# Optimization experiments

Hardware: AMD Instinct MI355X
Metric: run time of the kernel (lower is better)

The kernel has to match this reference:

```python
import jax, jax.numpy as jnp
import numpy as np

# Standard genetic code: 64 codons ordered by bases T,C,A,G (first/second/third position).
AA64 = "FFLLSSSSYY**CC*WLLLLPPPPHHQQRRRRIIIMTTTTNNKKSSRRVVVVAAAADDEEGGGG"
NC = 65  # codon vocab: id 0 = PAD, ids 1..64 = codons
_uniq = sorted(set(AA64))
_gid = {a: i + 1 for i, a in enumerate(_uniq)}          # group 0 reserved for PAD
NG = len(_uniq) + 1                                      # number of AA groups (+dummy)
GROUP_IDS = jnp.asarray(np.array([0] + [_gid[a] for a in AA64], dtype=np.int32))
IS_CODING = jnp.asarray(np.array([False] + [a != '*' for a in AA64]))
_syn = {a: AA64.count(a) for a in _uniq}
NSYN = jnp.asarray(np.array([0.0] + [float(_syn[a]) for a in AA64], dtype=np.float32))

LOSS_W = dict(ce=1.0, cai=0.4, rscu=0.3, gc=0.1, structure=0.15, dynamics=0.1)
EPS = 1e-8


def _cai(codon_ids, species_ids, mask, weight_matrix):
    # per-token gather of CAI weights: [B, L]
    w = weight_matrix[species_ids[:, None], codon_ids]
    log_w = jnp.log(jnp.maximum(w, EPS))
    m = mask.astype(log_w.dtype)
    mean_log = (log_w * m).sum(1) / jnp.maximum(m.sum(1), 1.0)
    return jnp.exp(mean_log)  # [B]


def _seq_rscu(codon_ids, aa_ids, mask):
    # grouped codon histogram -> RSCU: count * n_syn(aa) / total_count(aa)
    B = codon_ids.shape[0]
    bi = jnp.arange(B)[:, None]
    valid = mask & (codon_ids > 0)
    counts = jnp.zeros((B, NC), jnp.float32).at[bi, codon_ids].add(valid.astype(jnp.float32))
    aa_valid = valid & (aa_ids > 2)  # positions with a real amino-acid token
    observed = jnp.zeros((B, NC), jnp.float32).at[bi, codon_ids].add(aa_valid.astype(jnp.float32)) > 0
    observed = observed & IS_CODING[None, :]
    obs_counts = counts * observed  # counts of codons observed under a valid AA
    # segment-sum over synonymous-codon groups
    group_sum = jnp.zeros((B, NG), jnp.float32).at[:, GROUP_IDS].add(obs_counts)
    tot = group_sum[:, GROUP_IDS]  # [B, NC] total count of each codon's syn group
    return jnp.where(observed & (tot > 0), obs_counts * NSYN[None, :] / jnp.maximum(tot, 1.0), 0.0)


def _rscu_kl(pred_ids, target_ids, aa_ids, species_ids, mask, ref_distributions):
    pred_rscu = _seq_rscu(pred_ids, aa_ids, mask)
    target_rscu = _seq_rscu(target_ids, aa_ids, mask)
    ref_rscu = ref_distributions[species_ids]  # [B, NC]
    combined = 0.7 * target_rscu + 0.3 * ref_rscu + EPS
    pred = pred_rscu + EPS
    p = pred / pred.sum(1, keepdims=True)
    t = combined / combined.sum(1, keepdims=True)
    return (t * (jnp.log(t) - jnp.log(p))).sum(1)  # [B]


def setup_inputs() -> dict:
    key = jax.random.key(0)
    ks = jax.random.split(key, 9)
    B, L = 64, 8192
    return {
        "logits": jax.random.normal(ks[0], (B, L, NC), jnp.float32),
        "weight_matrix": jax.random.uniform(ks[1], (5, NC), jnp.float32),
        "ref_distributions": jax.random.uniform(ks[2], (5, NC), jnp.float32) * 2.0,
        "gc_pred": jax.random.uniform(ks[3], (B, L), jnp.float32),
        "mfe": jax.random.normal(ks[4], (B,), jnp.float32) * 5.0 - 20.0,
        "pause_prob": jax.random.uniform(ks[5], (B, L), jnp.float32),
        "target_codon_ids": jax.random.randint(ks[6], (B, L), 0, NC),
        "aa_ids": jax.random.randint(ks[7], (B, L), 0, 25),
        "species_ids": jax.random.randint(ks[8], (B,), 0, 5),
        "mask": jnp.ones((B, L), dtype=bool),
    }


def reference(logits, weight_matrix, ref_distributions, gc_pred, mfe, pause_prob,
              target_codon_ids, aa_ids, species_ids, mask):
    # CE with ignore_index=0
    logp = jax.nn.log_softmax(logits, axis=-1)
    nll = -jnp.take_along_axis(logp, target_codon_ids[..., None], axis=-1)[..., 0]
    v = (target_codon_ids != 0).astype(logits.dtype)
    ce = (nll * v).sum() / jnp.maximum(v.sum(), 1.0)

    pred_ids = jnp.argmax(logits, axis=-1)

    pred_cai = _cai(pred_ids, species_ids, mask, weight_matrix)
    target_cai = _cai(target_codon_ids, species_ids, mask, weight_matrix)
    cai_loss = jax.nn.relu(target_cai - pred_cai).mean()

    rscu_loss = _rscu_kl(pred_ids, target_codon_ids, aa_ids, species_ids, mask, ref_distributions).mean()

    gc_loss = jnp.mean((gc_pred.mean(1) - 0.5) ** 2)
    structure_loss = jnp.mean((mfe - (-20.0)) ** 2)
    dynamics_loss = jnp.mean((pause_prob.mean(1) - 0.1) ** 2)

    total = (LOSS_W['ce'] * ce + LOSS_W['cai'] * cai_loss + LOSS_W['rscu'] * rscu_loss
             + LOSS_W['gc'] * gc_loss + LOSS_W['structure'] * structure_loss
             + LOSS_W['dynamics'] * dynamics_loss)
    return total
```

## Files before the change

kernel.cpp:

```cpp
#include <hip/hip_runtime.h>
#include <math.h>
#include <stdint.h>

#define NCC 65
#define NGG 22
#define BB  64
#define LL  8192
#define EPSF 1e-8f
#define TPB 128
#define PPB 128
#define TILES 4
#define SUBS 16
#define NBLK (BB * SUBS)

__device__ __constant__ int c_gid[NCC] = {0,
  6,6,11,11,17,17,17,17,21,21,1,1,3,3,1,20,
  11,11,11,11,14,14,14,14,8,8,15,15,16,16,16,16,
  9,9,9,12,18,18,18,18,13,13,10,10,17,17,16,16,
  19,19,19,19,2,2,2,2,4,4,5,5,7,7,7,7};
__device__ __constant__ int c_coding[NCC] = {0,
  1,1,1,1,1,1,1,1,1,1,0,0,1,1,0,1,
  1,1,1,1,1,1,1,1,1,1,1,1,1,1,1,1,
  1,1,1,1,1,1,1,1,1,1,1,1,1,1,1,1,
  1,1,1,1,1,1,1,1,1,1,1,1,1,1,1,1};
__device__ __constant__ float c_nsyn[NCC] = {0.f,
  2,2,6,6,6,6,6,6,2,2,3,3,2,2,3,1,
  6,6,6,6,4,4,4,4,2,2,2,2,6,6,6,6,
  3,3,3,1,4,4,4,4,2,2,2,2,6,6,6,6,
  4,4,4,4,4,4,4,4,2,2,2,2,4,4,4,4};

#define WS_NLL  0
#define WS_VC   64
#define WS_LWP  128
#define WS_LWT  192
#define WS_G    256
#define WS_P    320
#define WS_PART 384
#define WS_HIST 448

__global__ __launch_bounds__(TPB) void k_main(
    const float* __restrict__ logits, const float* __restrict__ wmat,
    const float* __restrict__ gcp,    const float* __restrict__ ppr,
    const int* __restrict__ tgt,      const int* __restrict__ aa,
    const int* __restrict__ spec,     float* __restrict__ ws)
{
  const int b    = blockIdx.x >> 4;
  const int sub  = blockIdx.x & (SUBS - 1);
  const int tid  = threadIdx.x;
  const int lane = tid & 63;

  __shared__ float tile[PPB * NCC];
  __shared__ float lwrow[NCC];
  __shared__ int hPV[NCC], hPA[NCC], hTV[NCC], hTA[NCC];

  const int sp = spec[b];
  if (tid < NCC) {
    hPV[tid] = 0; hPA[tid] = 0; hTV[tid] = 0; hTA[tid] = 0;
    lwrow[tid] = logf(fmaxf(wmat[sp * NCC + tid], EPSF));
  }

  float nll = 0.f, vc = 0.f, lwp = 0.f, lwt = 0.f, g = 0.f, p = 0.f;

  const int posBase0 = sub * (TILES * PPB);

  for (int tl = 0; tl < TILES; tl++) {
    const int posBase = posBase0 + tl * PPB;
    const size_t gposBase = (size_t)b * LL + posBase;

    if (tl) __syncthreads();
    {
      const float4* src = (const float4*)(logits + gposBase * NCC);
      float4* dst = (float4*)tile;
      for (int i = tid; i < PPB * NCC / 4; i += TPB) dst[i] = src[i];
    }
    __syncthreads();

    const size_t gpos = gposBase + tid;
    g += gcp[gpos];
    p += ppr[gpos];
    const int t = tgt[gpos];
    const int q = aa[gpos];
    const int base = tid * NCC;

    float m = tile[base];
    int am = 0;
    #pragma unroll 8
    for (int c = 1; c < NCC; c++) {
      float x = tile[base + c];
      if (x > m) { m = x; am = c; }
    }
    float s0 = 0.f, s1 = 0.f;
    #pragma unroll 8
    for (int c = 0; c < NCC - 1; c += 2) {
      s0 += __expf(tile[base + c]     - m);
      s1 += __expf(tile[base + c + 1] - m);
    }
    float s = s0 + s1 + __expf(tile[base + NCC - 1] - m);
    float lse = m + __logf(s);
    float xt  = tile[base + t];

    if (t != 0) {
      nll += lse - xt; vc += 1.f;
      atomicAdd(&hTV[t], 1);
      if (q > 2) atomicAdd(&hTA[t], 1);
    }
    const int pred = am;
    if (pred != 0) {
      atomicAdd(&hPV[pred], 1);
      if (q > 2) atomicAdd(&hPA[pred], 1);
    }
    lwt += lwrow[t];
    lwp += lwrow[pred];
  }

  #pragma unroll
  for (int off = 32; off; off >>= 1) {
    nll += __shfl_xor(nll, off);
    vc  += __shfl_xor(vc,  off);
    lwp += __shfl_xor(lwp, off);
    lwt += __shfl_xor(lwt, off);
    g   += __shfl_xor(g,   off);
    p   += __shfl_xor(p,   off);
  }
  if (lane == 0) {
    atomicAdd(&ws[WS_NLL + b], nll);
    atomicAdd(&ws[WS_VC  + b], vc);
    atomicAdd(&ws[WS_LWP + b], lwp);
    atomicAdd(&ws[WS_LWT + b], lwt);
    atomicAdd(&ws[WS_G   + b], g);
    atomicAdd(&ws[WS_P   + b], p);
  }

  __syncthreads();
  int* P = (int*)(ws + WS_HIST) + (size_t)blockIdx.x * 260;
  for (int c = tid; c < NCC; c += TPB) {
    P[          c] = hPV[c];
    P[    NCC + c] = hPA[c];
    P[2 * NCC + c] = hTV[c];
    P[3 * NCC + c] = hTA[c];
  }
}

__global__ __launch_bounds__(64) void k_final(
    const float* __restrict__ refd, const float* __restrict__ mfe,
    const int* __restrict__ spec,   float* __restrict__ ws)
{
  const int b = blockIdx.x;
  const int lane = threadIdx.x;
  const int sp = spec[b];

  __shared__ int sH[4 * NCC];
  __shared__ float gsP[NGG], gsT[NGG];
  if (lane < NGG) { gsP[lane] = 0.f; gsT[lane] = 0.f; }

  const int* P = (const int*)(ws + WS_HIST);
  for (int idx = lane; idx < 4 * NCC; idx += 64) {
    int s = 0;
    #pragma unroll
    for (int k = 0; k < SUBS; k++)
      s += P[((size_t)(b * SUBS + k)) * 260 + idx];
    sH[idx] = s;
  }
  __syncthreads();

  const int   cs[2]  = {lane, 64};
  const bool  act[2] = {true, lane == 0};
  float ocP[2], ocT[2];
  int   obP[2], obT[2];

  #pragma unroll
  for (int k = 0; k < 2; k++) {
    ocP[k] = 0.f; ocT[k] = 0.f; obP[k] = 0; obT[k] = 0;
    if (act[k]) {
      const int c = cs[k];
      int hv = sH[          c];
      int ha = sH[    NCC + c];
      obP[k] = (ha > 0) && c_coding[c];
      ocP[k] = obP[k] ? (float)hv : 0.f;
      if (ocP[k] != 0.f) atomicAdd(&gsP[c_gid[c]], ocP[k]);
      hv = sH[2 * NCC + c];
      ha = sH[3 * NCC + c];
      obT[k] = (ha > 0) && c_coding[c];
      ocT[k] = obT[k] ? (float)hv : 0.f;
      if (ocT[k] != 0.f) atomicAdd(&gsT[c_gid[c]], ocT[k]);
    }
  }
  __syncthreads();

  float pv[2], tv[2];
  float psum = 0.f, tsum = 0.f;
  #pragma unroll
  for (int k = 0; k < 2; k++) {
    pv[k] = 0.f; tv[k] = 0.f;
    if (act[k]) {
      const int c = cs[k];
      float totP = gsP[c_gid[c]];
      float rP = (obP[k] && totP > 0.f) ? ocP[k] * c_nsyn[c] / fmaxf(totP, 1.f) : 0.f;
      float totT = gsT[c_gid[c]];
      float rT = (obT[k] && totT > 0.f) ? ocT[k] * c_nsyn[c] / fmaxf(totT, 1.f) : 0.f;
      pv[k] = rP + EPSF;
      tv[k] = 0.7f * rT + 0.3f * refd[sp * NCC + c] + EPSF;
      psum += pv[k]; tsum += tv[k];
    }
  }
  #pragma unroll
  for (int off = 32; off; off >>= 1) {
    psum += __shfl_xor(psum, off);
    tsum += __shfl_xor(tsum, off);
  }
  float kl = 0.f;
  #pragma unroll
  for (int k = 0; k < 2; k++) {
    if (act[k]) {
      float pn = pv[k] / psum;
      float tn = tv[k] / tsum;
      kl += tn * (logf(tn) - logf(pn));
    }
  }
  #pragma unroll
  for (int off = 32; off; off >>= 1) kl += __shfl_xor(kl, off);

  if (lane == 0) {
    float pred_cai = expf(ws[WS_LWP + b] * (1.f / (float)LL));
    float tgt_cai  = expf(ws[WS_LWT + b] * (1.f / (float)LL));
    float cai_t = fmaxf(tgt_cai - pred_cai, 0.f);
    float gc_t = ws[WS_G + b] * (1.f / (float)LL) - 0.5f; gc_t *= gc_t;
    float ps_t = ws[WS_P + b] * (1.f / (float)LL) - 0.1f; ps_t *= ps_t;
    float mf   = mfe[b] + 20.f;
    float mf_t = mf * mf;

    float inv = 1.f / (float)BB;
    ws[WS_PART + b] = 0.4f  * cai_t * inv
                    + 0.3f  * kl    * inv
                    + 0.1f  * gc_t  * inv
                    + 0.15f * mf_t  * inv
                    + 0.1f  * ps_t  * inv;
  }
}

__global__ __launch_bounds__(64) void k_sum(const float* __restrict__ ws,
                                            float* __restrict__ out)
{
  const int b = threadIdx.x;
  float part = ws[WS_PART + b];
  float nll  = ws[WS_NLL + b];
  float vc   = ws[WS_VC  + b];
  #pragma unroll
  for (int off = 32; off; off >>= 1) {
    part += __shfl_xor(part, off);
    nll  += __shfl_xor(nll,  off);
    vc   += __shfl_xor(vc,   off);
  }
  if (b == 0) out[0] = part + nll / fmaxf(vc, 1.f);
}

extern "C" void kernel_launch(void* const* d_in, const int* in_sizes, int n_in,
                              void* d_out, int out_size, void* d_ws, size_t ws_size,
                              hipStream_t stream) {
  const float* logits = (const float*)d_in[0];
  const float* wmat   = (const float*)d_in[1];
  const float* refd   = (const float*)d_in[2];
  const float* gcp    = (const float*)d_in[3];
  const float* mfe    = (const float*)d_in[4];
  const float* ppr    = (const float*)d_in[5];
  const int*   tgt    = (const int*)d_in[6];
  const int*   aa     = (const int*)d_in[7];
  const int*   spec   = (const int*)d_in[8];
  float* ws = (float*)d_ws;

  hipMemsetAsync(d_ws, 0, WS_PART * sizeof(float), stream);

  k_main<<<dim3(NBLK), dim3(TPB), 0, stream>>>(logits, wmat, gcp, ppr,
                                               tgt, aa, spec, ws);
  k_final<<<dim3(BB), dim3(64), 0, stream>>>(refd, mfe, spec, ws);
  k_sum<<<dim3(1), dim3(64), 0, stream>>>(ws, (float*)d_out);
}
```

Baseline: 245.3 us.

## Halve block size, double sub-blocks, register-cache logits, store uint16 histograms

Measured after the change: 233.4 us. -4.9%, faster.

```diff
diff --git a/kernel.cpp b/kernel.cpp
--- a/kernel.cpp
+++ b/kernel.cpp
@@ -7,10 +7,10 @@
 #define BB  64
 #define LL  8192
 #define EPSF 1e-8f
-#define TPB 128
-#define PPB 128
+#define TPB 64
+#define PPB 64
 #define TILES 4
-#define SUBS 16
+#define SUBS 32
 #define NBLK (BB * SUBS)
 
 __device__ __constant__ int c_gid[NCC] = {0,
@@ -36,7 +36,7 @@
 #define WS_G    256
 #define WS_P    320
 #define WS_PART 384
-#define WS_HIST 448
+#define WS_HIST_BYTES 1792
 
 __global__ __launch_bounds__(TPB) void k_main(
     const float* __restrict__ logits, const float* __restrict__ wmat,
@@ -44,34 +44,34 @@
     const int* __restrict__ tgt,      const int* __restrict__ aa,
     const int* __restrict__ spec,     float* __restrict__ ws)
 {
-  const int b    = blockIdx.x >> 4;
-  const int sub  = blockIdx.x & (SUBS - 1);
-  const int tid  = threadIdx.x;
-  const int lane = tid & 63;
+  const int b   = blockIdx.x >> 5;
+  const int sub = blockIdx.x & (SUBS - 1);
+  const int tid = threadIdx.x;
 
   __shared__ float tile[PPB * NCC];
   __shared__ float lwrow[NCC];
-  __shared__ int hPV[NCC], hPA[NCC], hTV[NCC], hTA[NCC];
+  __shared__ int   sh[4 * NCC];
 
   const int sp = spec[b];
-  if (tid < NCC) {
-    hPV[tid] = 0; hPA[tid] = 0; hTV[tid] = 0; hTA[tid] = 0;
-    lwrow[tid] = logf(fmaxf(wmat[sp * NCC + tid], EPSF));
-  }
+  lwrow[tid] = logf(fmaxf(wmat[sp * NCC + tid], EPSF));
+  if (tid == 0) lwrow[64] = logf(fmaxf(wmat[sp * NCC + 64], EPSF));
+  #pragma unroll
+  for (int i = tid; i < 4 * NCC; i += TPB) sh[i] = 0;
 
   float nll = 0.f, vc = 0.f, lwp = 0.f, lwt = 0.f, g = 0.f, p = 0.f;
 
-  const int posBase0 = sub * (TILES * PPB);
+  const int posB0 = sub * (TILES * PPB);
 
   for (int tl = 0; tl < TILES; tl++) {
-    const int posBase = posBase0 + tl * PPB;
-    const size_t gposBase = (size_t)b * LL + posBase;
-
-    if (tl) __syncthreads();
+    const size_t gposBase = (size_t)b * LL + posB0 + tl * PPB;
+
+    __syncthreads();
     {
       const float4* src = (const float4*)(logits + gposBase * NCC);
       float4* dst = (float4*)tile;
-      for (int i = tid; i < PPB * NCC / 4; i += TPB) dst[i] = src[i];
+      #pragma unroll
+      for (int j = 0; j < 16; j++) dst[j * 64 + tid] = src[j * 64 + tid];
+      dst[976 + tid] = src[976 + tid];
     }
     __syncthreads();
 
@@ -82,35 +82,38 @@
     const int q = aa[gpos];
     const int base = tid * NCC;
 
-    float m = tile[base];
-    int am = 0;
-    #pragma unroll 8
+    float r[NCC];
+    #pragma unroll
+    for (int c = 0; c < NCC; c++) r[c] = tile[base + c];
+
+    float m = r[0]; int am = 0;
+    #pragma unroll
     for (int c = 1; c < NCC; c++) {
-      float x = tile[base + c];
-      if (x > m) { m = x; am = c; }
-    }
-    float s0 = 0.f, s1 = 0.f;
-    #pragma unroll 8
-    for (int c = 0; c < NCC - 1; c += 2) {
-      s0 += __expf(tile[base + c]     - m);
-      s1 += __expf(tile[base + c + 1] - m);
-    }
-    float s = s0 + s1 + __expf(tile[base + NCC - 1] - m);
+      if (r[c] > m) { m = r[c]; am = c; }
+    }
+    float s0 = 0.f, s1 = 0.f, s2 = 0.f, s3 = 0.f;
+    #pragma unroll
+    for (int c = 0; c < 64; c += 4) {
+      s0 += __expf(r[c]     - m);
+      s1 += __expf(r[c + 1] - m);
+      s2 += __expf(r[c + 2] - m);
+      s3 += __expf(r[c + 3] - m);
+    }
+    float s = (s0 + s1) + (s2 + s3) + __expf(r[64] - m);
     float lse = m + __logf(s);
     float xt  = tile[base + t];
 
     if (t != 0) {
       nll += lse - xt; vc += 1.f;
-      atomicAdd(&hTV[t], 1);
-      if (q > 2) atomicAdd(&hTA[t], 1);
-    }
-    const int pred = am;
-    if (pred != 0) {
-      atomicAdd(&hPV[pred], 1);
-      if (q > 2) atomicAdd(&hPA[pred], 1);
+      atomicAdd(&sh[130 + t], 1);
+      if (q > 2) atomicAdd(&sh[195 + t], 1);
+    }
+    if (am != 0) {
+      atomicAdd(&sh[am], 1);
+      if (q > 2) atomicAdd(&sh[65 + am], 1);
     }
     lwt += lwrow[t];
-    lwp += lwrow[pred];
+    lwp += lwrow[am];
   }
 
   #pragma unroll
@@ -122,7 +125,7 @@
     g   += __shfl_xor(g,   off);
     p   += __shfl_xor(p,   off);
   }
-  if (lane == 0) {
+  if (tid == 0) {
     atomicAdd(&ws[WS_NLL + b], nll);
     atomicAdd(&ws[WS_VC  + b], vc);
     atomicAdd(&ws[WS_LWP + b], lwp);
@@ -132,13 +135,10 @@
   }
 
   __syncthreads();
-  int* P = (int*)(ws + WS_HIST) + (size_t)blockIdx.x * 260;
-  for (int c = tid; c < NCC; c += TPB) {
-    P[          c] = hPV[c];
-    P[    NCC + c] = hPA[c];
-    P[2 * NCC + c] = hTV[c];
-    P[3 * NCC + c] = hTA[c];
-  }
+  unsigned short* P = (unsigned short*)((char*)ws + WS_HIST_BYTES)
+                    + (size_t)blockIdx.x * 260;
+  #pragma unroll
+  for (int i = tid; i < 4 * NCC; i += TPB) P[i] = (unsigned short)sh[i];
 }
 
 __global__ __launch_bounds__(64) void k_final(
@@ -153,12 +153,12 @@
   __shared__ float gsP[NGG], gsT[NGG];
   if (lane < NGG) { gsP[lane] = 0.f; gsT[lane] = 0.f; }
 
-  const int* P = (const int*)(ws + WS_HIST);
+  const unsigned short* P = (const unsigned short*)((const char*)ws + WS_HIST_BYTES);
   for (int idx = lane; idx < 4 * NCC; idx += 64) {
     int s = 0;
     #pragma unroll
     for (int k = 0; k < SUBS; k++)
-      s += P[((size_t)(b * SUBS + k)) * 260 + idx];
+      s += P[(size_t)(b * SUBS + k) * 260 + idx];
     sH[idx] = s;
   }
   __syncthreads();
```
